# Performance work log

Measured on AMD Instinct MI355X. Metric: run time of the kernel, lower is better.

## Reference

```python
import jax, jax.numpy as jnp
import numpy as np

WINDOW = 512  # window_size from init_kwargs


def _sliding_window_attn(q, k, v, window):
    # q,k,v: [B, S, H, D]; each query attends to keys j with i-window < j <= i (causal band)
    B, S, H, D = q.shape
    W = window
    NB = S // W  # S chosen divisible by W
    qb = q.reshape(B, NB, W, H, D)
    kb = k.reshape(B, NB, W, H, D)
    vb = v.reshape(B, NB, W, H, D)
    # previous block of keys/values (zeros for block 0, masked out below)
    kprev = jnp.pad(kb, ((0, 0), (1, 0), (0, 0), (0, 0), (0, 0)))[:, :NB]
    vprev = jnp.pad(vb, ((0, 0), (1, 0), (0, 0), (0, 0), (0, 0)))[:, :NB]
    kcat = jnp.concatenate([kprev, kb], axis=2)  # [B, NB, 2W, H, D]
    vcat = jnp.concatenate([vprev, vb], axis=2)
    qi = jnp.arange(W)
    kj = jnp.arange(2 * W) - W  # key position relative to block start
    rel = kj[None, :] - qi[:, None]  # [W, 2W]
    win_mask = (rel <= 0) & (rel > -W)  # causal window of size W (incl. self)
    blk = jnp.arange(NB)
    valid_key = (blk[:, None, None] > 0) | (kj[None, None, :] >= 0)  # block 0 has no prev
    mask = win_mask[None] & valid_key  # [NB, W, 2W]
    scale = 1.0 / np.sqrt(D).astype(np.float32)
    scores = jnp.einsum('bnqhd,bnkhd->bhnqk', qb, kcat) * scale  # [B,H,NB,W,2W]
    scores = jnp.where(mask[None, None], scores, jnp.finfo(scores.dtype).min)
    probs = jax.nn.softmax(scores, axis=-1)
    out = jnp.einsum('bhnqk,bnkhd->bnqhd', probs, vcat)  # [B,NB,W,H,D]
    return out.reshape(B, S, H, D)


def setup_inputs() -> dict:
    B, S, H, D = 2, 8192, 8, 64
    root = jax.random.key(0)
    k1, k2, k3, k4, k5 = jax.random.split(root, 5)
    query = jax.random.normal(k1, (B, S, H, D), dtype=jnp.float32)
    key = jax.random.normal(k2, (B, S, H, D), dtype=jnp.float32)
    value = jax.random.normal(k3, (B, S, H, D), dtype=jnp.float32)
    W_out = jax.random.normal(k4, (H * D, H * D), dtype=jnp.float32) * (1.0 / np.sqrt(H * D))
    b_out = jax.random.normal(k5, (H * D,), dtype=jnp.float32) * 0.01
    return {'query': query, 'key': key, 'value': value, 'W_out': W_out, 'b_out': b_out}


def reference(query, key, value, W_out, b_out):
    B, S, H, D = query.shape
    # seq_len (8192) > window_size (512) -> sliding-window branch of the module
    attn = _sliding_window_attn(query, key, value, WINDOW)
    flat = attn.reshape(B, S, H * D)
    # out_proj (nn.Linear); dropout=0.0 is identity; no attention_mask
    return flat @ W_out.T + b_out
```

## Files before the change

kernel.cpp:

```cpp
#include <hip/hip_runtime.h>

#define B_ 2
#define S_ 8192
#define H_ 8
#define D_ 64
#define HD_ 512
#define WIN_ 512

typedef __bf16 bf16x8 __attribute__((ext_vector_type(8)));
typedef float f32x4 __attribute__((ext_vector_type(4)));
typedef unsigned short u16;
typedef unsigned int u32;

__device__ __forceinline__ u16 f2bf(float f) {
  u32 u = __float_as_uint(f);
  u += 0x7FFFu + ((u >> 16) & 1u);
  return (u16)(u >> 16);
}

__device__ __forceinline__ bf16x8 cvt8s(const float* p, float s) {
  const float4 a = *(const float4*)p;
  const float4 b = *(const float4*)(p + 4);
  union { u16 s[8]; bf16x8 v; } r;
  r.s[0] = f2bf(a.x * s); r.s[1] = f2bf(a.y * s); r.s[2] = f2bf(a.z * s); r.s[3] = f2bf(a.w * s);
  r.s[4] = f2bf(b.x * s); r.s[5] = f2bf(b.y * s); r.s[6] = f2bf(b.z * s); r.s[7] = f2bf(b.w * s);
  return r.v;
}

#define MFMA(a, b, c) __builtin_amdgcn_mfma_f32_16x16x32_bf16(a, b, c, 0, 0, 0)

__global__ __launch_bounds__(256) void cvt_kernel(const float* __restrict__ in,
                                                  u16* __restrict__ out, int n4) {
  int i = blockIdx.x * 256 + threadIdx.x;
  if (i < n4) {
    float4 f = ((const float4*)in)[i];
    ushort4 r;
    r.x = f2bf(f.x); r.y = f2bf(f.y); r.z = f2bf(f.z); r.w = f2bf(f.w);
    ((ushort4*)out)[i] = r;
  }
}

__global__ __launch_bounds__(512) void attn_kernel(const float* __restrict__ q,
                                                   const float* __restrict__ kf,
                                                   const float* __restrict__ vf,
                                                   u16* __restrict__ attn) {
  const int tid = threadIdx.x;
  const int lane = tid & 63;
  const int wave = tid >> 6;
  const int lg = lane >> 4;
  const int lj = lane & 15;
  const int bid = (int)blockIdx.x;
  const int swz = (bid & 7) * 128 + (bid >> 3);
  const int qc = swz & 63;
  const int bh = swz >> 6;
  const int b = bh >> 3, h = bh & 7;
  const int q0blk = qc * 128;
  const int q0w = q0blk + wave * 16;

  __shared__ __align__(16) u16 klds0[32 * 64], klds1[32 * 64];
  __shared__ __align__(16) u16 vlds0[64 * 32], vlds1[64 * 32];
  __shared__ __align__(16) u16 plds[8][16 * 40];

  const float qscale = 0.125f * 1.4426950408889634f;
  bf16x8 aq0, aq1;
  {
    const float* qrow = q + ((size_t)(b * S_ + q0w + lj) * H_ + h) * D_;
    aq0 = cvt8s(qrow + lg * 8, qscale);
    aq1 = cvt8s(qrow + 32 + lg * 8, qscale);
  }

  f32x4 o0 = {0.f, 0.f, 0.f, 0.f}, o1 = o0, o2 = o0, o3 = o0;
  float lacc[4] = {0.f, 0.f, 0.f, 0.f};

  const int tbw = (q0w >= WIN_) ? ((q0w - (WIN_ - 1)) >> 5) : 0;
  const int tew = (q0w + 15) >> 5;
  const int tbu = (q0blk >= WIN_) ? ((q0blk - (WIN_ - 1)) >> 5) : 0;
  const int teu = (q0blk + 127) >> 5;
  const bool wmask = (q0w >= WIN_);

  const bool isK = (wave < 4);
  const float* gf;
  const size_t gstepf = (size_t)32 * H_ * D_;
  u16 *l0, *l1;
  int vkey = 0, vd0 = 0;
  if (isK) {
    const int chunk = wave * 64 + lane;
    const int r = chunk >> 3, c = chunk & 7;
    gf = kf + ((size_t)(b * S_ + r) * H_ + h) * D_ + c * 8;
    const int dst = r * 64 + ((c * 8) ^ ((r & 7) << 3));
    l0 = klds0 + dst; l1 = klds1 + dst;
  } else {
    const int u = (wave - 4) * 64 + lane;
    vkey = u & 31;
    vd0 = (u >> 5) * 8;
    gf = vf + ((size_t)(b * S_ + vkey) * H_ + h) * D_ + vd0;
    l0 = vlds0; l1 = vlds1;
  }

  auto kpack = [](float4 a, float4 c) {
    union { u16 s[8]; uint4 q; } t;
    t.s[0] = f2bf(a.x); t.s[1] = f2bf(a.y); t.s[2] = f2bf(a.z); t.s[3] = f2bf(a.w);
    t.s[4] = f2bf(c.x); t.s[5] = f2bf(c.y); t.s[6] = f2bf(c.z); t.s[7] = f2bf(c.w);
    return t.q;
  };
  auto vscatter = [&](u16* vb, float4 a, float4 c) {
    float vals[8] = {a.x, a.y, a.z, a.w, c.x, c.y, c.z, c.w};
#pragma unroll
    for (int i = 0; i < 8; ++i) {
      const int d = vd0 + i;
      vb[d * 32 + (vkey ^ ((d & 3) << 3))] = f2bf(vals[i]);
    }
  };

  const int ko0 = lj * 64 + ((lg * 8) ^ ((lj & 7) << 3));
  const int ko1 = lj * 64 + (((32 + lg * 8)) ^ ((lj & 7) << 3));
  const int vo = lj * 32 + ((lg * 8) ^ ((lj & 3) << 3));
  const int po = lj * 40 + lg * 8;

  {
    float4 a = *(const float4*)(gf + gstepf * tbu);
    float4 c = *(const float4*)(gf + gstepf * tbu + 4);
    if (isK) *(uint4*)l0 = kpack(a, c);
    else vscatter(vlds0, a, c);
  }
  float4 ga, gb;
  if (tbu < teu) {
    ga = *(const float4*)(gf + gstepf * (tbu + 1));
    gb = *(const float4*)(gf + gstepf * (tbu + 1) + 4);
  }
  __syncthreads();

  int cur = 0;
  for (int t = tbu; t <= teu; ++t) {
    if (t >= tbw && t <= tew) {
      const u16* K = cur ? klds1 : klds0;
      const u16* V = cur ? vlds1 : vlds0;
      bf16x8 k00 = *(const bf16x8*)(K + ko0);
      bf16x8 k01 = *(const bf16x8*)(K + ko1);
      bf16x8 k10 = *(const bf16x8*)(K + ko0 + 1024);
      bf16x8 k11 = *(const bf16x8*)(K + ko1 + 1024);

      f32x4 sA = {0.f, 0.f, 0.f, 0.f}, sB = sA;
      sA = MFMA(aq0, k00, sA);
      sA = MFMA(aq1, k01, sA);
      sB = MFMA(aq0, k10, sB);
      sB = MFMA(aq1, k11, sB);

      const bool edge = (t == tew) || (wmask && t == tbw);
      u16* ps = &plds[wave][0];
#pragma unroll
      for (int r = 0; r < 4; ++r) {
        float ea = __builtin_amdgcn_exp2f(sA[r]);
        float eb = __builtin_amdgcn_exp2f(sB[r]);
        if (edge) {
          const int qpos = q0w + lg * 4 + r;
          const int kA = 32 * t + lj, kB = kA + 16;
          const bool okA = (kA <= qpos) && (kA > qpos - WIN_);
          const bool okB = (kB <= qpos) && (kB > qpos - WIN_);
          ea = okA ? ea : 0.f;
          eb = okB ? eb : 0.f;
        }
        lacc[r] += ea + eb;
        ps[(lg * 4 + r) * 40 + lj] = (u16)(__float_as_uint(ea) >> 16);
        ps[(lg * 4 + r) * 40 + 16 + lj] = (u16)(__float_as_uint(eb) >> 16);
      }
      bf16x8 ap = *(const bf16x8*)(ps + po);

      bf16x8 v0 = *(const bf16x8*)(V + vo);
      bf16x8 v1 = *(const bf16x8*)(V + vo + 512);
      bf16x8 v2 = *(const bf16x8*)(V + vo + 1024);
      bf16x8 v3 = *(const bf16x8*)(V + vo + 1536);
      o0 = MFMA(ap, v0, o0);
      o1 = MFMA(ap, v1, o1);
      o2 = MFMA(ap, v2, o2);
      o3 = MFMA(ap, v3, o3);
    }

    if (t < teu) {
      if (isK) {
        u16* dst = cur ? l0 : l1;
        *(uint4*)dst = kpack(ga, gb);
      } else {
        vscatter(cur ? vlds0 : vlds1, ga, gb);
      }
    }
    __syncthreads();
    if (t + 1 < teu) {
      ga = *(const float4*)(gf + gstepf * (t + 2));
      gb = *(const float4*)(gf + gstepf * (t + 2) + 4);
    }
    cur ^= 1;
  }

#pragma unroll
  for (int r = 0; r < 4; ++r) {
    float l = lacc[r];
    l += __shfl_xor(l, 1);
    l += __shfl_xor(l, 2);
    l += __shfl_xor(l, 4);
    l += __shfl_xor(l, 8);
    const float inv = 1.0f / l;
    const int row = q0w + lg * 4 + r;
    u16* orow = attn + (size_t)(b * S_ + row) * HD_ + h * D_;
    orow[lj] = f2bf(o0[r] * inv);
    orow[16 + lj] = f2bf(o1[r] * inv);
    orow[32 + lj] = f2bf(o2[r] * inv);
    orow[48 + lj] = f2bf(o3[r] * inv);
  }
}

__global__ __launch_bounds__(512) void gemm_kernel(const u16* __restrict__ A,
                                                   const u16* __restrict__ Wb,
                                                   const float* __restrict__ bias,
                                                   float* __restrict__ out) {
  const int tid = threadIdx.x;
  const int lane = tid & 63;
  const int wave = tid >> 6;
  const int lg = lane >> 4, lj = lane & 15;
  const int phys = (int)blockIdx.x;
  const int swz = (phys & 7) * 32 + (phys >> 3);
  const int rb = swz >> 1, cb = swz & 1;
  const int wr = wave >> 2, wc = wave & 3;
  const int row0 = rb * 128;
  const int col0 = cb * 256 + wc * 64;

  __shared__ __align__(16) u16 alds[2][128 * 64];

  const int srow = tid >> 3;
  const int skc = tid & 7;
  const u16* ag0 = A + (size_t)(row0 + srow) * HD_ + skc * 8;
  const u16* ag1 = A + (size_t)(row0 + 64 + srow) * HD_ + skc * 8;
  const int dst0 = srow * 64 + ((skc * 8) ^ ((srow & 7) << 3));
  const int dst1 = (64 + srow) * 64 + ((skc * 8) ^ ((srow & 7) << 3));

  f32x4 acc[4][4];
#pragma unroll
  for (int fr = 0; fr < 4; ++fr)
#pragma unroll
    for (int fc = 0; fc < 4; ++fc) acc[fr][fc] = (f32x4){0.f, 0.f, 0.f, 0.f};

  *(uint4*)(&alds[0][dst0]) = *(const uint4*)ag0;
  *(uint4*)(&alds[0][dst1]) = *(const uint4*)ag1;
  __syncthreads();

  uint4 pre0, pre1;
  int cur = 0;
  for (int kt = 0; kt < HD_; kt += 64) {
    if (kt + 64 < HD_) {
      pre0 = *(const uint4*)(ag0 + kt + 64);
      pre1 = *(const uint4*)(ag1 + kt + 64);
    }
    const u16* Abuf = alds[cur];
#pragma unroll
    for (int ks = 0; ks < 2; ++ks) {
      bf16x8 fa[4], fb[4];
#pragma unroll
      for (int fr = 0; fr < 4; ++fr) {
        const int rr = wr * 64 + fr * 16 + lj;
        fa[fr] = *(const bf16x8*)(Abuf + rr * 64 + ((ks * 32 + lg * 8) ^ ((lj & 7) << 3)));
      }
#pragma unroll
      for (int fc = 0; fc < 4; ++fc)
        fb[fc] = *(const bf16x8*)(Wb + (size_t)(col0 + fc * 16 + lj) * HD_ + kt + ks * 32 + lg * 8);
#pragma unroll
      for (int fr = 0; fr < 4; ++fr)
#pragma unroll
        for (int fc = 0; fc < 4; ++fc)
          acc[fr][fc] = MFMA(fa[fr], fb[fc], acc[fr][fc]);
    }
    if (kt + 64 < HD_) {
      u16* db = alds[cur ^ 1];
      *(uint4*)(&db[dst0]) = pre0;
      *(uint4*)(&db[dst1]) = pre1;
    }
    __syncthreads();
    cur ^= 1;
  }

#pragma unroll
  for (int fc = 0; fc < 4; ++fc) {
    const float bv = bias[col0 + fc * 16 + lj];
#pragma unroll
    for (int fr = 0; fr < 4; ++fr) {
#pragma unroll
      for (int r = 0; r < 4; ++r) {
        const int row = row0 + wr * 64 + fr * 16 + lg * 4 + r;
        out[(size_t)row * HD_ + col0 + fc * 16 + lj] = acc[fr][fc][r] + bv;
      }
    }
  }
}

extern "C" void kernel_launch(void* const* d_in, const int* in_sizes, int n_in,
                              void* d_out, int out_size, void* d_ws, size_t ws_size,
                              hipStream_t stream) {
  const float* q = (const float*)d_in[0];
  const float* k = (const float*)d_in[1];
  const float* v = (const float*)d_in[2];
  const float* w = (const float*)d_in[3];
  const float* bias = (const float*)d_in[4];
  float* out = (float*)d_out;

  char* ws = (char*)d_ws;
  u16* attn = (u16*)ws;
  u16* wb = (u16*)(ws + 16777216);

  hipLaunchKernelGGL(cvt_kernel, dim3(256), dim3(256), 0, stream, w, wb, 65536);
  hipLaunchKernelGGL(attn_kernel, dim3(1024), dim3(512), 0, stream, q, k, v, attn);
  hipLaunchKernelGGL(gemm_kernel, dim3(256), dim3(512), 0, stream, attn, wb, bias, out);
}
```

Baseline: 85.53 us.

## Process two 16-row query subtiles per wave to reuse K/V tiles

Each wave now handles 32 query rows as two 16-row subtiles, so each block covers 256 queries and the grid is halved. K/V tiles loaded into LDS and fragments read per step are reused across both subtiles, which cuts global loads and staging per query. The cost is more registers for the doubled accumulators and Q fragments, fewer blocks in flight, and the shared P scratch buffer being reused back to back by the two subtiles.

```diff
diff --git a/kernel.cpp b/kernel.cpp
--- a/kernel.cpp
+++ b/kernel.cpp
@@ -50,33 +50,44 @@
   const int lg = lane >> 4;
   const int lj = lane & 15;
   const int bid = (int)blockIdx.x;
-  const int swz = (bid & 7) * 128 + (bid >> 3);
-  const int qc = swz & 63;
-  const int bh = swz >> 6;
+  const int swz = (bid & 7) * 64 + (bid >> 3);
+  const int qc = swz & 31;
+  const int bh = swz >> 5;
   const int b = bh >> 3, h = bh & 7;
-  const int q0blk = qc * 128;
-  const int q0w = q0blk + wave * 16;
+  const int q0blk = qc * 256;
+  const int q0w = q0blk + wave * 32;
 
   __shared__ __align__(16) u16 klds0[32 * 64], klds1[32 * 64];
   __shared__ __align__(16) u16 vlds0[64 * 32], vlds1[64 * 32];
   __shared__ __align__(16) u16 plds[8][16 * 40];
 
   const float qscale = 0.125f * 1.4426950408889634f;
-  bf16x8 aq0, aq1;
-  {
-    const float* qrow = q + ((size_t)(b * S_ + q0w + lj) * H_ + h) * D_;
-    aq0 = cvt8s(qrow + lg * 8, qscale);
-    aq1 = cvt8s(qrow + 32 + lg * 8, qscale);
-  }
-
-  f32x4 o0 = {0.f, 0.f, 0.f, 0.f}, o1 = o0, o2 = o0, o3 = o0;
-  float lacc[4] = {0.f, 0.f, 0.f, 0.f};
-
-  const int tbw = (q0w >= WIN_) ? ((q0w - (WIN_ - 1)) >> 5) : 0;
-  const int tew = (q0w + 15) >> 5;
+  bf16x8 aq[2][2];
+#pragma unroll
+  for (int qs = 0; qs < 2; ++qs) {
+    const float* qrow = q + ((size_t)(b * S_ + q0w + qs * 16 + lj) * H_ + h) * D_;
+    aq[qs][0] = cvt8s(qrow + lg * 8, qscale);
+    aq[qs][1] = cvt8s(qrow + 32 + lg * 8, qscale);
+  }
+
+  f32x4 o[2][4];
+#pragma unroll
+  for (int qs = 0; qs < 2; ++qs)
+#pragma unroll
+    for (int g = 0; g < 4; ++g) o[qs][g] = (f32x4){0.f, 0.f, 0.f, 0.f};
+  float lacc[2][4] = {};
+
+  const int te_w = q0w >> 5;
+  int tbq[2];
+  bool wm[2];
+#pragma unroll
+  for (int qs = 0; qs < 2; ++qs) {
+    const int qq = q0w + qs * 16;
+    wm[qs] = (qq >= WIN_);
+    tbq[qs] = wm[qs] ? ((qq - (WIN_ - 1)) >> 5) : 0;
+  }
   const int tbu = (q0blk >= WIN_) ? ((q0blk - (WIN_ - 1)) >> 5) : 0;
-  const int teu = (q0blk + 127) >> 5;
-  const bool wmask = (q0w >= WIN_);
+  const int teu = (q0blk + 255) >> 5;
 
   const bool isK = (wave < 4);
   const float* gf;
@@ -132,48 +143,51 @@
 
   int cur = 0;
   for (int t = tbu; t <= teu; ++t) {
-    if (t >= tbw && t <= tew) {
+    if (t >= tbq[0] && t <= te_w) {
       const u16* K = cur ? klds1 : klds0;
       const u16* V = cur ? vlds1 : vlds0;
       bf16x8 k00 = *(const bf16x8*)(K + ko0);
       bf16x8 k01 = *(const bf16x8*)(K + ko1);
       bf16x8 k10 = *(const bf16x8*)(K + ko0 + 1024);
       bf16x8 k11 = *(const bf16x8*)(K + ko1 + 1024);
-
-      f32x4 sA = {0.f, 0.f, 0.f, 0.f}, sB = sA;
-      sA = MFMA(aq0, k00, sA);
-      sA = MFMA(aq1, k01, sA);
-      sB = MFMA(aq0, k10, sB);
-      sB = MFMA(aq1, k11, sB);
-
-      const bool edge = (t == tew) || (wmask && t == tbw);
-      u16* ps = &plds[wave][0];
-#pragma unroll
-      for (int r = 0; r < 4; ++r) {
-        float ea = __builtin_amdgcn_exp2f(sA[r]);
-        float eb = __builtin_amdgcn_exp2f(sB[r]);
-        if (edge) {
-          const int qpos = q0w + lg * 4 + r;
-          const int kA = 32 * t + lj, kB = kA + 16;
-          const bool okA = (kA <= qpos) && (kA > qpos - WIN_);
-          const bool okB = (kB <= qpos) && (kB > qpos - WIN_);
-          ea = okA ? ea : 0.f;
-          eb = okB ? eb : 0.f;
-        }
-        lacc[r] += ea + eb;
-        ps[(lg * 4 + r) * 40 + lj] = (u16)(__float_as_uint(ea) >> 16);
-        ps[(lg * 4 + r) * 40 + 16 + lj] = (u16)(__float_as_uint(eb) >> 16);
-      }
-      bf16x8 ap = *(const bf16x8*)(ps + po);
-
       bf16x8 v0 = *(const bf16x8*)(V + vo);
       bf16x8 v1 = *(const bf16x8*)(V + vo + 512);
       bf16x8 v2 = *(const bf16x8*)(V + vo + 1024);
       bf16x8 v3 = *(const bf16x8*)(V + vo + 1536);
-      o0 = MFMA(ap, v0, o0);
-      o1 = MFMA(ap, v1, o1);
-      o2 = MFMA(ap, v2, o2);
-      o3 = MFMA(ap, v3, o3);
+
+#pragma unroll
+      for (int qs = 0; qs < 2; ++qs) {
+        if (t < tbq[qs]) continue;
+        f32x4 sA = {0.f, 0.f, 0.f, 0.f}, sB = sA;
+        sA = MFMA(aq[qs][0], k00, sA);
+        sA = MFMA(aq[qs][1], k01, sA);
+        sB = MFMA(aq[qs][0], k10, sB);
+        sB = MFMA(aq[qs][1], k11, sB);
+
+        const bool edge = (t == te_w) || (wm[qs] && t == tbq[qs]);
+        u16* ps = &plds[wave][0];
+#pragma unroll
+        for (int r = 0; r < 4; ++r) {
+          float ea = __builtin_amdgcn_exp2f(sA[r]);
+          float eb = __builtin_amdgcn_exp2f(sB[r]);
+          if (edge) {
+            const int qpos = q0w + qs * 16 + lg * 4 + r;
+            const int kA = 32 * t + lj, kB = kA + 16;
+            const bool okA = (kA <= qpos) && (kA > qpos - WIN_);
+            const bool okB = (kB <= qpos) && (kB > qpos - WIN_);
+            ea = okA ? ea : 0.f;
+            eb = okB ? eb : 0.f;
+          }
+          lacc[qs][r] += ea + eb;
+          ps[(lg * 4 + r) * 40 + lj] = (u16)(__float_as_uint(ea) >> 16);
+          ps[(lg * 4 + r) * 40 + 16 + lj] = (u16)(__float_as_uint(eb) >> 16);
+        }
+        bf16x8 ap = *(const bf16x8*)(ps + po);
+        o[qs][0] = MFMA(ap, v0, o[qs][0]);
+        o[qs][1] = MFMA(ap, v1, o[qs][1]);
+        o[qs][2] = MFMA(ap, v2, o[qs][2]);
+        o[qs][3] = MFMA(ap, v3, o[qs][3]);
+      }
     }
 
     if (t < teu) {
@@ -193,19 +207,22 @@
   }
 
 #pragma unroll
-  for (int r = 0; r < 4; ++r) {
-    float l = lacc[r];
-    l += __shfl_xor(l, 1);
-    l += __shfl_xor(l, 2);
-    l += __shfl_xor(l, 4);
-    l += __shfl_xor(l, 8);
-    const float inv = 1.0f / l;
-    const int row = q0w + lg * 4 + r;
-    u16* orow = attn + (size_t)(b * S_ + row) * HD_ + h * D_;
-    orow[lj] = f2bf(o0[r] * inv);
-    orow[16 + lj] = f2bf(o1[r] * inv);
-    orow[32 + lj] = f2bf(o2[r] * inv);
-    orow[48 + lj] = f2bf(o3[r] * inv);
+  for (int qs = 0; qs < 2; ++qs) {
+#pragma unroll
+    for (int r = 0; r < 4; ++r) {
+      float l = lacc[qs][r];
+      l += __shfl_xor(l, 1);
+      l += __shfl_xor(l, 2);
+      l += __shfl_xor(l, 4);
+      l += __shfl_xor(l, 8);
+      const float inv = 1.0f / l;
+      const int row = q0w + qs * 16 + lg * 4 + r;
+      u16* orow = attn + (size_t)(b * S_ + row) * HD_ + h * D_;
+      orow[lj] = f2bf(o[qs][0][r] * inv);
+      orow[16 + lj] = f2bf(o[qs][1][r] * inv);
+      orow[32 + lj] = f2bf(o[qs][2][r] * inv);
+      orow[48 + lj] = f2bf(o[qs][3][r] * inv);
+    }
   }
 }
 
@@ -306,6 +323,6 @@
   u16* wb = (u16*)(ws + 16777216);
 
   hipLaunchKernelGGL(cvt_kernel, dim3(256), dim3(256), 0, stream, w, wb, 65536);
-  hipLaunchKernelGGL(attn_kernel, dim3(1024), dim3(512), 0, stream, q, k, v, attn);
+  hipLaunchKernelGGL(attn_kernel, dim3(512), dim3(512), 0, stream, q, k, v, attn);
   hipLaunchKernelGGL(gemm_kernel, dim3(256), dim3(512), 0, stream, attn, wb, bias, out);
 }
```

After: 94.84 us. 10.9% more time.
